# Optimization experiments

Measured on AMD Instinct MI355X. Metric: run time of the kernel, lower is better.

## Reference

```python
import jax, jax.numpy as jnp
import numpy as np

N_NODES = 100000
N_EDGES = 1600000
D_IN = 128
D_HID = 128
D_OUT = 32


def setup_inputs() -> dict:
    key = jax.random.key(0)
    ks = jax.random.split(key, 10)
    x = jax.random.normal(ks[0], (N_NODES, D_IN), dtype=jnp.float32)
    edge_index = jax.random.randint(ks[1], (2, N_EDGES), 0, N_NODES, dtype=jnp.int64)
    s = 0.05
    return {
        "x": x,
        "edge_index": edge_index,
        "Wl0": jax.random.normal(ks[2], (D_IN, D_HID), jnp.float32) * s,
        "bl0": jnp.zeros((D_HID,), jnp.float32),
        "Wr0": jax.random.normal(ks[3], (D_IN, D_HID), jnp.float32) * s,
        "Wl1": jax.random.normal(ks[4], (D_HID, D_HID), jnp.float32) * s,
        "bl1": jnp.zeros((D_HID,), jnp.float32),
        "Wr1": jax.random.normal(ks[5], (D_HID, D_HID), jnp.float32) * s,
        "Wl2": jax.random.normal(ks[6], (D_HID, D_OUT), jnp.float32) * s,
        "bl2": jnp.zeros((D_OUT,), jnp.float32),
        "Wr2": jax.random.normal(ks[7], (D_HID, D_OUT), jnp.float32) * s,
    }


def _sage_conv(x, src, dst, Wl, bl, Wr):
    # PyG SAGEConv (aggr='mean', root_weight=True):
    # out[i] = lin_l(mean_{j in N(i)} x_j) + lin_r(x_i)
    n = x.shape[0]
    msgs = x[src]                                        # [E, F] gather
    agg = jax.ops.segment_sum(msgs, dst, num_segments=n) # [N, F] scatter-add
    deg = jax.ops.segment_sum(jnp.ones((src.shape[0],), x.dtype), dst, num_segments=n)
    mean = agg / jnp.maximum(deg, 1.0)[:, None]
    return mean @ Wl + bl + x @ Wr


def reference(x, edge_index, Wl0, bl0, Wr0, Wl1, bl1, Wr1, Wl2, bl2, Wr2):
    src, dst = edge_index[0], edge_index[1]
    h = jax.nn.relu(_sage_conv(x, src, dst, Wl0, bl0, Wr0))
    h = jax.nn.relu(_sage_conv(h, src, dst, Wl1, bl1, Wr1))
    h = _sage_conv(h, src, dst, Wl2, bl2, Wr2)
    return jax.nn.log_softmax(h, axis=1)
```

## Files before the change

kernel.cpp:

```cpp
#include <hip/hip_runtime.h>
#include <hip/hip_bf16.h>
#include <math.h>

#define NN 100000
#define NE 1600000

#define NCB 391
#define EB  4096
#define SCT 512
#define EPT 8
#define HBK 64
#define NSB 391
#define WPB 144

typedef __attribute__((ext_vector_type(8))) short short8;
typedef __attribute__((ext_vector_type(4))) float f32x4;

__device__ __forceinline__ unsigned short f2bf(float f) {
  union { float f; unsigned int i; } v; v.f = f;
  unsigned int i = v.i;
  unsigned int r = (i + 0x7FFFu + ((i >> 16) & 1u)) >> 16;
  return (unsigned short)r;
}
__device__ __forceinline__ float bflo(unsigned int u) {
  union { unsigned int i; float f; } v; v.i = u << 16; return v.f;
}
__device__ __forceinline__ float bfhi(unsigned int u) {
  union { unsigned int i; float f; } v; v.i = u & 0xFFFF0000u; return v.f;
}
__device__ __forceinline__ float bf1(unsigned short u) {
  union { unsigned int i; float f; } v; v.i = ((unsigned int)u) << 16; return v.f;
}

__global__ __launch_bounds__(512) void k_prep(
    const int* __restrict__ dst, int* __restrict__ part,
    const float* __restrict__ Wl0, const float* __restrict__ Wr0,
    const float* __restrict__ Wl1, const float* __restrict__ Wr1,
    const float* __restrict__ Wl2, const float* __restrict__ Wr2,
    unsigned short* __restrict__ B0, unsigned short* __restrict__ B1,
    unsigned short* __restrict__ B2) {
  if (blockIdx.x < HBK) {
    __shared__ int h[NCB];
    for (int i = threadIdx.x; i < NCB; i += 512) h[i] = 0;
    __syncthreads();
    int stride = HBK * 512;
    for (int e = blockIdx.x * 512 + threadIdx.x; e < NE; e += stride) {
      int d = dst[e];
      d = d < 0 ? 0 : (d >= NN ? NN - 1 : d);
      atomicAdd(&h[d >> 8], 1);
    }
    __syncthreads();
    for (int i = threadIdx.x; i < NCB; i += 512) part[blockIdx.x * NCB + i] = h[i];
  } else {
    int idx = (blockIdx.x - HBK) * 512 + threadIdx.x;
    if (idx < 32768) {
      int n = idx >> 7, k = idx & 127;
      float v = (n < 128) ? Wl0[k * 128 + n] : Wr0[k * 128 + (n - 128)];
      B0[idx] = f2bf(v);
    } else if (idx < 65536) {
      int j = idx - 32768;
      int n = j >> 7, k = j & 127;
      float v = (n < 128) ? Wl1[k * 128 + n] : Wr1[k * 128 + (n - 128)];
      B1[j] = f2bf(v);
    } else if (idx < 73728) {
      int j = idx - 65536;
      int n = j >> 7, k = j & 127;
      float v = (n < 32) ? Wl2[k * 32 + n] : Wr2[k * 32 + (n - 32)];
      B2[j] = f2bf(v);
    }
  }
}

__global__ __launch_bounds__(512) void k_cscan(const int* __restrict__ part,
                                               int* __restrict__ cboff,
                                               int* __restrict__ ccur,
                                               int* __restrict__ csroff) {
  __shared__ int sd[512];
  int t = threadIdx.x;
  int v = 0;
  if (t < NCB) {
    int s0 = 0, s1 = 0, s2 = 0, s3 = 0;
    #pragma unroll 4
    for (int k = 0; k < HBK; k += 4) {
      s0 += part[(k + 0) * NCB + t];
      s1 += part[(k + 1) * NCB + t];
      s2 += part[(k + 2) * NCB + t];
      s3 += part[(k + 3) * NCB + t];
    }
    v = (s0 + s1) + (s2 + s3);
    ccur[t * 16] = 0;
  }
  sd[t] = v;
  __syncthreads();
  for (int st = 1; st < 512; st <<= 1) {
    int x = (t >= st) ? sd[t - st] : 0;
    __syncthreads();
    sd[t] += x;
    __syncthreads();
  }
  if (t < NCB) cboff[t] = sd[t] - v;
  if (t == NCB - 1) { cboff[NCB] = sd[t]; csroff[NN] = sd[t]; }
}


__device__ __forceinline__ void cscatter_body(
    char* smem, int bid,
    const int* __restrict__ src, const int* __restrict__ dst,
    const int* __restrict__ cboff, int* __restrict__ ccur,
    unsigned int* __restrict__ ebuf) {
  int* lh = (int*)smem;
  int t = threadIdx.x;
  int base = bid * EB;
  for (int i = t; i < NCB; i += SCT) lh[i] = 0;
  __syncthreads();
  unsigned int rk[EPT], pv[EPT];
  #pragma unroll
  for (int i = 0; i < EPT; i++) {
    int e = base + i * SCT + t;
    rk[i] = 0xFFFFFFFFu;
    pv[i] = 0;
    if (e < NE) {
      int d = dst[e];
      d = d < 0 ? 0 : (d >= NN ? NN - 1 : d);
      int s = src[e];
      s = s < 0 ? 0 : (s >= NN ? NN - 1 : s);
      int cb = d >> 8;
      int r = atomicAdd(&lh[cb], 1);
      rk[i] = (((unsigned int)cb) << 13) | (unsigned int)r;
      pv[i] = (((unsigned int)(d & 255)) << 17) | (unsigned int)s;
    }
  }
  __syncthreads();
  for (int i = t; i < NCB; i += SCT) {
    int c = lh[i];
    int g = c ? atomicAdd(&ccur[i * 16], c) : 0;
    lh[i] = cboff[i] + g;
  }
  __syncthreads();
  #pragma unroll
  for (int i = 0; i < EPT; i++) {
    unsigned int r = rk[i];
    if (r != 0xFFFFFFFFu) {
      ebuf[lh[r >> 13] + (r & 0x1FFF)] = pv[i];
    }
  }
}

__device__ __forceinline__ void mgemm0_body(
    char* smem, int bid, const float* __restrict__ A,
    const unsigned short* __restrict__ Bp, const float* __restrict__ bias,
    unsigned short* __restrict__ yl, unsigned short* __restrict__ yr) {
  unsigned short* sA = (unsigned short*)smem;
  int tid = threadIdx.x;
  int nb  = bid * 128;

  #pragma unroll
  for (int i = 0; i < 8; i++) {
    int j = i * 512 + tid;
    int m = j >> 5;
    int k4 = (j & 31) * 4;
    int gn = nb + m;
    float4 v = make_float4(0.f, 0.f, 0.f, 0.f);
    if (gn < NN) v = *(const float4*)&A[gn * 128 + k4];
    unsigned int p0 = (unsigned int)f2bf(v.x) | ((unsigned int)f2bf(v.y) << 16);
    unsigned int p1 = (unsigned int)f2bf(v.z) | ((unsigned int)f2bf(v.w) << 16);
    *(uint2*)&sA[m * 136 + k4] = make_uint2(p0, p1);
  }
  __syncthreads();

  int wave = tid >> 6, lane = tid & 63;
  int l15 = lane & 15, lq = lane >> 4;
  int wm = wave & 1, wn = wave >> 1;
  int mbase = wm * 64;
  int nbase = wn * 64;

  f32x4 acc[4][4];
  #pragma unroll
  for (int mi = 0; mi < 4; mi++)
    #pragma unroll
    for (int ni = 0; ni < 4; ni++) acc[mi][ni] = (f32x4){0.f, 0.f, 0.f, 0.f};

  #pragma unroll
  for (int kc = 0; kc < 4; kc++) {
    int k0 = kc * 32 + lq * 8;
    short8 af[4], bfr[4];
    #pragma unroll
    for (int ni = 0; ni < 4; ni++)
      bfr[ni] = *(const short8*)&Bp[(nbase + ni * 16 + l15) * 128 + k0];
    #pragma unroll
    for (int mi = 0; mi < 4; mi++)
      af[mi] = *(const short8*)&sA[(mbase + mi * 16 + l15) * 136 + k0];
    #pragma unroll
    for (int mi = 0; mi < 4; mi++)
      #pragma unroll
      for (int ni = 0; ni < 4; ni++)
        acc[mi][ni] = __builtin_amdgcn_mfma_f32_16x16x32_bf16(
            af[mi], bfr[ni], acc[mi][ni], 0, 0, 0);
  }

  #pragma unroll
  for (int mi = 0; mi < 4; mi++) {
    #pragma unroll
    for (int ni = 0; ni < 4; ni++) {
      int n = nbase + ni * 16 + l15;
      #pragma unroll
      for (int r = 0; r < 4; r++) {
        int gn = nb + mbase + mi * 16 + lq * 4 + r;
        if (gn < NN) {
          float v = acc[mi][ni][r];
          if (n < 128) {
            yl[(size_t)gn * 128 + n] = f2bf(v);
          } else {
            int n2 = n - 128;
            yr[(size_t)gn * 128 + n2] = f2bf(v + bias[n2]);
          }
        }
      }
    }
  }
}

__global__ __launch_bounds__(512, 4) void k_scatgemm(
    const int* __restrict__ src, const int* __restrict__ dst,
    const int* __restrict__ cboff, int* __restrict__ ccur,
    unsigned int* __restrict__ ebuf,
    const float* __restrict__ x, const unsigned short* __restrict__ B0,
    const float* __restrict__ bias,
    unsigned short* __restrict__ yl, unsigned short* __restrict__ yr) {
  __shared__ char smem[128 * 136 * 2];
  if (blockIdx.x < NSB) {
    cscatter_body(smem, blockIdx.x, src, dst, cboff, ccur, ebuf);
  } else {
    mgemm0_body(smem, blockIdx.x - NSB, x, B0, bias, yl, yr);
  }
}

__global__ __launch_bounds__(256) void k_crefine(
    const unsigned int* __restrict__ ebuf, const int* __restrict__ cboff,
    int* __restrict__ csroff, float* __restrict__ invd,
    int* __restrict__ csrsrc) {
  __shared__ int lh[256], pos[256], cur[256];
  int b = blockIdx.x, t = threadIdx.x;
  lh[t] = 0; cur[t] = 0;
  __syncthreads();
  int beg = cboff[b], end = cboff[b + 1];
  for (int i = beg + t; i < end; i += 256) atomicAdd(&lh[ebuf[i] >> 17], 1);
  __syncthreads();
  int v = lh[t];
  pos[t] = v;
  __syncthreads();
  for (int st = 1; st < 256; st <<= 1) {
    int x = (t >= st) ? pos[t - st] : 0;
    __syncthreads();
    pos[t] += x;
    __syncthreads();
  }
  int nid = b * 256 + t;
  int mybase = cboff[b] + pos[t] - v;
  if (nid < NN) {
    csroff[nid] = mybase;
    invd[nid] = 1.0f / (float)(v < 1 ? 1 : v);
  }
  __syncthreads();
  pos[t] = mybase;
  __syncthreads();
  for (int i = beg + t; i < end; i += 256) {
    unsigned int u = ebuf[i];
    int local = u >> 17;
    int r = atomicAdd(&cur[local], 1);
    csrsrc[pos[local] + r] = (int)(u & 0x1FFFFu);
  }
}

template <int NC>
__global__ __launch_bounds__(512) void k_mgemm(
    const unsigned short* __restrict__ A, const unsigned short* __restrict__ Bp,
    const float* __restrict__ bias,
    unsigned short* __restrict__ yl, unsigned short* __restrict__ yr) {
  __shared__ unsigned short sA[128 * 136];
  int tid = threadIdx.x;
  int nb  = blockIdx.x * 128;

  #pragma unroll
  for (int i = 0; i < 4; i++) {
    int j = i * 512 + tid;
    int m = j >> 4;
    int k8 = (j & 15) * 8;
    int gn = nb + m;
    uint4 v = make_uint4(0, 0, 0, 0);
    if (gn < NN) v = *(const uint4*)&A[gn * 128 + k8];
    *(uint4*)&sA[m * 136 + k8] = v;
  }
  __syncthreads();

  int wave = tid >> 6, lane = tid & 63;
  int l15 = lane & 15, lq = lane >> 4;
  constexpr int MT = (NC == 256) ? 4 : 2;
  constexpr int NT = (NC == 256) ? 4 : 2;
  int wm, wn;
  if (NC == 256) { wm = wave & 1; wn = wave >> 1; }
  else           { wm = wave >> 1; wn = wave & 1; }
  int mbase = wm * (MT * 16);
  int nbase = wn * (NT * 16);

  f32x4 acc[MT][NT];
  #pragma unroll
  for (int mi = 0; mi < MT; mi++)
    #pragma unroll
    for (int ni = 0; ni < NT; ni++) acc[mi][ni] = (f32x4){0.f, 0.f, 0.f, 0.f};

  #pragma unroll
  for (int kc = 0; kc < 4; kc++) {
    int k0 = kc * 32 + lq * 8;
    short8 af[MT], bfr[NT];
    #pragma unroll
    for (int ni = 0; ni < NT; ni++)
      bfr[ni] = *(const short8*)&Bp[(nbase + ni * 16 + l15) * 128 + k0];
    #pragma unroll
    for (int mi = 0; mi < MT; mi++)
      af[mi] = *(const short8*)&sA[(mbase + mi * 16 + l15) * 136 + k0];
    #pragma unroll
    for (int mi = 0; mi < MT; mi++)
      #pragma unroll
      for (int ni = 0; ni < NT; ni++)
        acc[mi][ni] = __builtin_amdgcn_mfma_f32_16x16x32_bf16(
            af[mi], bfr[ni], acc[mi][ni], 0, 0, 0);
  }

  constexpr int HC = NC / 2;
  #pragma unroll
  for (int mi = 0; mi < MT; mi++) {
    #pragma unroll
    for (int ni = 0; ni < NT; ni++) {
      int n = nbase + ni * 16 + l15;
      #pragma unroll
      for (int r = 0; r < 4; r++) {
        int gn = nb + mbase + mi * 16 + lq * 4 + r;
        if (gn < NN) {
          float v = acc[mi][ni][r];
          if (n < HC) {
            yl[(size_t)gn * HC + n] = f2bf(v);
          } else {
            int n2 = n - HC;
            yr[(size_t)gn * HC + n2] = f2bf(v + bias[n2]);
          }
        }
      }
    }
  }
}

#define ACC8(u) do { \
  a0 += bflo((u).x); a1 += bfhi((u).x); \
  a2 += bflo((u).y); a3 += bfhi((u).y); \
  a4 += bflo((u).z); a5 += bfhi((u).z); \
  a6 += bflo((u).w); a7 += bfhi((u).w); } while (0)

__global__ __launch_bounds__(256) void k_agg128(
    const unsigned short* __restrict__ yl, const unsigned short* __restrict__ yr,
    const int* __restrict__ off, const int* __restrict__ csr,
    const float* __restrict__ invd, unsigned short* __restrict__ out, int relu) {
  int wid  = (blockIdx.x * 256 + threadIdx.x) >> 6;
  int lane = threadIdx.x & 63;
  if (wid >= NN) return;
  int beg = off[wid], end = off[wid + 1];
  int deg = end - beg;
  int q   = lane >> 4;
  int l16 = lane & 15;
  const uint4* ylp = (const uint4*)yl;

  float sc = invd[wid];
  uint4 rv = ((const uint4*)yr)[wid * 16 + l16];

  float a0 = 0.f, a1 = 0.f, a2 = 0.f, a3 = 0.f;
  float a4 = 0.f, a5 = 0.f, a6 = 0.f, a7 = 0.f;

  for (int w0 = 0; w0 < deg; w0 += 64) {
    int ei = w0 + lane;
    int sv = (ei < deg) ? csr[beg + ei] : 0;
    int wcnt = deg - w0; if (wcnt > 64) wcnt = 64;
    int full = wcnt >> 2;
    int p = 0;
    for (; p + 4 <= full; p += 4) {
      int b = p * 4 + q;
      int s0 = __shfl(sv, b,      64);
      int s1 = __shfl(sv, b + 4,  64);
      int s2 = __shfl(sv, b + 8,  64);
      int s3 = __shfl(sv, b + 12, 64);
      uint4 u0 = ylp[s0 * 16 + l16];
      uint4 u1 = ylp[s1 * 16 + l16];
      uint4 u2 = ylp[s2 * 16 + l16];
      uint4 u3 = ylp[s3 * 16 + l16];
      ACC8(u0); ACC8(u1); ACC8(u2); ACC8(u3);
    }
    for (; p < full; p++) {
      int s0 = __shfl(sv, p * 4 + q, 64);
      uint4 u0 = ylp[s0 * 16 + l16];
      ACC8(u0);
    }
    int rem = wcnt & 3;
    if (rem && q < rem) {
      int s0 = __shfl(sv, full * 4 + q, 64);
      uint4 u0 = ylp[s0 * 16 + l16];
      ACC8(u0);
    }
  }

  a0 += __shfl_xor(a0, 16, 64); a0 += __shfl_xor(a0, 32, 64);
  a1 += __shfl_xor(a1, 16, 64); a1 += __shfl_xor(a1, 32, 64);
  a2 += __shfl_xor(a2, 16, 64); a2 += __shfl_xor(a2, 32, 64);
  a3 += __shfl_xor(a3, 16, 64); a3 += __shfl_xor(a3, 32, 64);
  a4 += __shfl_xor(a4, 16, 64); a4 += __shfl_xor(a4, 32, 64);
  a5 += __shfl_xor(a5, 16, 64); a5 += __shfl_xor(a5, 32, 64);
  a6 += __shfl_xor(a6, 16, 64); a6 += __shfl_xor(a6, 32, 64);
  a7 += __shfl_xor(a7, 16, 64); a7 += __shfl_xor(a7, 32, 64);

  float v0 = a0 * sc + bflo(rv.x), v1 = a1 * sc + bfhi(rv.x);
  float v2 = a2 * sc + bflo(rv.y), v3 = a3 * sc + bfhi(rv.y);
  float v4 = a4 * sc + bflo(rv.z), v5 = a5 * sc + bfhi(rv.z);
  float v6 = a6 * sc + bflo(rv.w), v7 = a7 * sc + bfhi(rv.w);
  if (relu) {
    v0 = fmaxf(v0, 0.f); v1 = fmaxf(v1, 0.f);
    v2 = fmaxf(v2, 0.f); v3 = fmaxf(v3, 0.f);
    v4 = fmaxf(v4, 0.f); v5 = fmaxf(v5, 0.f);
    v6 = fmaxf(v6, 0.f); v7 = fmaxf(v7, 0.f);
  }
  if (q == 0) {
    unsigned int p0 = (unsigned int)f2bf(v0) | ((unsigned int)f2bf(v1) << 16);
    unsigned int p1 = (unsigned int)f2bf(v2) | ((unsigned int)f2bf(v3) << 16);
    unsigned int p2 = (unsigned int)f2bf(v4) | ((unsigned int)f2bf(v5) << 16);
    unsigned int p3 = (unsigned int)f2bf(v6) | ((unsigned int)f2bf(v7) << 16);
    ((uint4*)out)[wid * 16 + l16] = make_uint4(p0, p1, p2, p3);
  }
}

#define ACC4(u) do { \
  a0 += bflo((u).x); a1 += bfhi((u).x); \
  a2 += bflo((u).y); a3 += bfhi((u).y); } while (0)

__global__ __launch_bounds__(256) void k_agg32_lsm(
    const unsigned short* __restrict__ yl, const unsigned short* __restrict__ yr,
    const int* __restrict__ off, const int* __restrict__ csr,
    const float* __restrict__ invd, float* __restrict__ out) {
  int wid  = (blockIdx.x * 256 + threadIdx.x) >> 6;
  int lane = threadIdx.x & 63;
  if (wid >= NN) return;
  int beg = off[wid], end = off[wid + 1];
  int deg = end - beg;
  int q  = lane >> 3;
  int l8 = lane & 7;
  const uint2* ylp = (const uint2*)yl;

  float sc = invd[wid];
  uint2 rv = ((const uint2*)yr)[wid * 8 + l8];

  float a0 = 0.f, a1 = 0.f, a2 = 0.f, a3 = 0.f;

  for (int w0 = 0; w0 < deg; w0 += 64) {
    int ei = w0 + lane;
    int sv = (ei < deg) ? csr[beg + ei] : 0;
    int wcnt = deg - w0; if (wcnt > 64) wcnt = 64;
    int full = wcnt >> 3;
    int p = 0;
    for (; p + 2 <= full; p += 2) {
      int b = p * 8 + q;
      int s0 = __shfl(sv, b,     64);
      int s1 = __shfl(sv, b + 8, 64);
      uint2 u0 = ylp[s0 * 8 + l8];
      uint2 u1 = ylp[s1 * 8 + l8];
      ACC4(u0); ACC4(u1);
    }
    for (; p < full; p++) {
      int s0 = __shfl(sv, p * 8 + q, 64);
      uint2 u0 = ylp[s0 * 8 + l8];
      ACC4(u0);
    }
    int rem = wcnt & 7;
    if (rem && q < rem) {
      int s0 = __shfl(sv, full * 8 + q, 64);
      uint2 u0 = ylp[s0 * 8 + l8];
      ACC4(u0);
    }
  }

  a0 += __shfl_xor(a0, 8, 64); a0 += __shfl_xor(a0, 16, 64); a0 += __shfl_xor(a0, 32, 64);
  a1 += __shfl_xor(a1, 8, 64); a1 += __shfl_xor(a1, 16, 64); a1 += __shfl_xor(a1, 32, 64);
  a2 += __shfl_xor(a2, 8, 64); a2 += __shfl_xor(a2, 16, 64); a2 += __shfl_xor(a2, 32, 64);
  a3 += __shfl_xor(a3, 8, 64); a3 += __shfl_xor(a3, 16, 64); a3 += __shfl_xor(a3, 32, 64);

  float v0 = a0 * sc + bflo(rv.x), v1 = a1 * sc + bfhi(rv.x);
  float v2 = a2 * sc + bflo(rv.y), v3 = a3 * sc + bfhi(rv.y);

  float m = fmaxf(fmaxf(v0, v1), fmaxf(v2, v3));
  m = fmaxf(m, __shfl_xor(m, 1, 64));
  m = fmaxf(m, __shfl_xor(m, 2, 64));
  m = fmaxf(m, __shfl_xor(m, 4, 64));
  float e0 = expf(v0 - m), e1 = expf(v1 - m);
  float e2 = expf(v2 - m), e3 = expf(v3 - m);
  float s = (e0 + e1) + (e2 + e3);
  s += __shfl_xor(s, 1, 64);
  s += __shfl_xor(s, 2, 64);
  s += __shfl_xor(s, 4, 64);
  float ls = logf(s);
  if (q == 0) {
    float4 o = make_float4(v0 - m - ls, v1 - m - ls, v2 - m - ls, v3 - m - ls);
    ((float4*)out)[wid * 8 + l8] = o;
  }
}


extern "C" void kernel_launch(void* const* d_in, const int* in_sizes, int n_in,
                              void* d_out, int out_size, void* d_ws, size_t ws_size,
                              hipStream_t stream) {
  (void)in_sizes; (void)n_in; (void)out_size; (void)ws_size;
  const float* x   = (const float*)d_in[0];
  const int*   ei  = (const int*)d_in[1];
  const float* Wl0 = (const float*)d_in[2];
  const float* bl0 = (const float*)d_in[3];
  const float* Wr0 = (const float*)d_in[4];
  const float* Wl1 = (const float*)d_in[5];
  const float* bl1 = (const float*)d_in[6];
  const float* Wr1 = (const float*)d_in[7];
  const float* Wl2 = (const float*)d_in[8];
  const float* bl2 = (const float*)d_in[9];
  const float* Wr2 = (const float*)d_in[10];
  const int* srcI = ei;
  const int* dstI = ei + NE;

  char* w = (char*)d_ws;
  int*   cboff  = (int*)(w + (32 << 10));
  unsigned short* B0 = (unsigned short*)(w + (64 << 10));
  unsigned short* B1 = (unsigned short*)(w + (160 << 10));
  unsigned short* B2 = (unsigned short*)(w + (256 << 10));
  int*   part   = (int*)(w + (288 << 10));
  int*   ccur   = (int*)(w + (416 << 10));
  int*   csroff = (int*)(w + (512 << 10));
  float* invd   = (float*)(w + (1024 << 10));
  unsigned int* ebuf = (unsigned int*)(w + (size_t)(2) * 1024 * 1024);
  int*   csrsrc = (int*)(w + (size_t)(9) * 1024 * 1024);
  unsigned short* ylb = (unsigned short*)(w + (size_t)(16) * 1024 * 1024);
  unsigned short* yrb = (unsigned short*)(w + (size_t)(48) * 1024 * 1024);
  unsigned short* hb  = (unsigned short*)(w + (size_t)(80) * 1024 * 1024);

  dim3 gg((NN + 127) / 128);

  k_prep<<<HBK + WPB, 512, 0, stream>>>(dstI, part, Wl0, Wr0, Wl1, Wr1, Wl2, Wr2,
                                        B0, B1, B2);
  k_cscan<<<1, 512, 0, stream>>>(part, cboff, ccur, csroff);
  k_scatgemm<<<NSB + 782, 512, 0, stream>>>(srcI, dstI, cboff, ccur, ebuf,
                                            x, B0, bl0, ylb, yrb);
  k_crefine<<<NCB, 256, 0, stream>>>(ebuf, cboff, csroff, invd, csrsrc);
  k_agg128<<<(NN * 64) / 256, 256, 0, stream>>>(ylb, yrb, csroff, csrsrc, invd, hb, 1);
  k_mgemm<256><<<gg, 512, 0, stream>>>(hb, B1, bl1, ylb, yrb);
  k_agg128<<<(NN * 64) / 256, 256, 0, stream>>>(ylb, yrb, csroff, csrsrc, invd, hb, 1);
  k_mgemm<64><<<gg, 512, 0, stream>>>(hb, B2, bl2, ylb, yrb);
  k_agg32_lsm<<<(NN * 64) / 256, 256, 0, stream>>>(ylb, yrb, csroff, csrsrc, invd,
                                                   (float*)d_out);
}
```

Before: 417.5 us.

## Fuse neighbor aggregation into following GEMM and interleave scatter/GEMM blocks

Replaces the separate k_agg128 and k_mgemm launches with k_aggemm. Each block's waves gather and mean-aggregate 16 nodes apiece and write the ReLU'd bf16 rows straight into the shared-memory A tile before the MFMA GEMM. This removes the hidden-activation round trip through global memory and two kernel launches. The trade-off is fewer waves per node and serial per-wave node loops, which may expose gather latency. Separately, k_scatgemm now interleaves scatter and GEMM blocks (one of every three blocks scatters) so the two workloads run at the same time across the GPU.

After: 507.3 us. 21.5% more time.

```diff
diff --git a/kernel.cpp b/kernel.cpp
--- a/kernel.cpp
+++ b/kernel.cpp
@@ -12,6 +12,7 @@
 #define HBK 64
 #define NSB 391
 #define WPB 144
+#define NGB 782
 
 typedef __attribute__((ext_vector_type(8))) short short8;
 typedef __attribute__((ext_vector_type(4))) float f32x4;
@@ -228,10 +229,12 @@
     const float* __restrict__ bias,
     unsigned short* __restrict__ yl, unsigned short* __restrict__ yr) {
   __shared__ char smem[128 * 136 * 2];
-  if (blockIdx.x < NSB) {
-    cscatter_body(smem, blockIdx.x, src, dst, cboff, ccur, ebuf);
+  int bid = blockIdx.x;
+  int third = bid / 3;
+  if (bid - third * 3 == 0) {
+    cscatter_body(smem, third, src, dst, cboff, ccur, ebuf);
   } else {
-    mgemm0_body(smem, blockIdx.x - NSB, x, B0, bias, yl, yr);
+    mgemm0_body(smem, bid - third - 1, x, B0, bias, yl, yr);
   }
 }
 
@@ -272,28 +275,96 @@
   }
 }
 
+#define ACC8(u) do { \
+  a0 += bflo((u).x); a1 += bfhi((u).x); \
+  a2 += bflo((u).y); a3 += bfhi((u).y); \
+  a4 += bflo((u).z); a5 += bfhi((u).z); \
+  a6 += bflo((u).w); a7 += bfhi((u).w); } while (0)
+
 template <int NC>
-__global__ __launch_bounds__(512) void k_mgemm(
-    const unsigned short* __restrict__ A, const unsigned short* __restrict__ Bp,
-    const float* __restrict__ bias,
-    unsigned short* __restrict__ yl, unsigned short* __restrict__ yr) {
+__global__ __launch_bounds__(512) void k_aggemm(
+    const unsigned short* __restrict__ yl, const unsigned short* __restrict__ yrr,
+    const int* __restrict__ off, const int* __restrict__ csr,
+    const float* __restrict__ invd,
+    const unsigned short* __restrict__ Bp, const float* __restrict__ bias,
+    unsigned short* __restrict__ outl, unsigned short* __restrict__ outr) {
   __shared__ unsigned short sA[128 * 136];
-  int tid = threadIdx.x;
-  int nb  = blockIdx.x * 128;
-
-  #pragma unroll
-  for (int i = 0; i < 4; i++) {
-    int j = i * 512 + tid;
-    int m = j >> 4;
-    int k8 = (j & 15) * 8;
-    int gn = nb + m;
-    uint4 v = make_uint4(0, 0, 0, 0);
-    if (gn < NN) v = *(const uint4*)&A[gn * 128 + k8];
-    *(uint4*)&sA[m * 136 + k8] = v;
-  }
-  __syncthreads();
-
-  int wave = tid >> 6, lane = tid & 63;
+  int tid = threadIdx.x, wave = tid >> 6, lane = tid & 63;
+  int nb = blockIdx.x * 128;
+  int q = lane >> 4, l16 = lane & 15;
+  const uint4* ylp = (const uint4*)yl;
+
+  #pragma unroll 1
+  for (int j = 0; j < 16; j++) {
+    int m = wave * 16 + j;
+    int wid = nb + m;
+    float a0 = 0.f, a1 = 0.f, a2 = 0.f, a3 = 0.f;
+    float a4 = 0.f, a5 = 0.f, a6 = 0.f, a7 = 0.f;
+    float sc = 0.f;
+    uint4 rv = make_uint4(0, 0, 0, 0);
+    if (wid < NN) {
+      sc = invd[wid];
+      rv = ((const uint4*)yrr)[wid * 16 + l16];
+      int beg = off[wid], end = off[wid + 1];
+      int deg = end - beg;
+      for (int w0 = 0; w0 < deg; w0 += 64) {
+        int ei = w0 + lane;
+        int sv = (ei < deg) ? csr[beg + ei] : 0;
+        int wcnt = deg - w0; if (wcnt > 64) wcnt = 64;
+        int full = wcnt >> 2;
+        int p = 0;
+        for (; p + 4 <= full; p += 4) {
+          int b = p * 4 + q;
+          int s0 = __shfl(sv, b,      64);
+          int s1 = __shfl(sv, b + 4,  64);
+          int s2 = __shfl(sv, b + 8,  64);
+          int s3 = __shfl(sv, b + 12, 64);
+          uint4 u0 = ylp[s0 * 16 + l16];
+          uint4 u1 = ylp[s1 * 16 + l16];
+          uint4 u2 = ylp[s2 * 16 + l16];
+          uint4 u3 = ylp[s3 * 16 + l16];
+          ACC8(u0); ACC8(u1); ACC8(u2); ACC8(u3);
+        }
+        for (; p < full; p++) {
+          int s0 = __shfl(sv, p * 4 + q, 64);
+          uint4 u0 = ylp[s0 * 16 + l16];
+          ACC8(u0);
+        }
+        int rem = wcnt & 3;
+        if (rem && q < rem) {
+          int s0 = __shfl(sv, full * 4 + q, 64);
+          uint4 u0 = ylp[s0 * 16 + l16];
+          ACC8(u0);
+        }
+      }
+    }
+    a0 += __shfl_xor(a0, 16, 64); a0 += __shfl_xor(a0, 32, 64);
+    a1 += __shfl_xor(a1, 16, 64); a1 += __shfl_xor(a1, 32, 64);
+    a2 += __shfl_xor(a2, 16, 64); a2 += __shfl_xor(a2, 32, 64);
+    a3 += __shfl_xor(a3, 16, 64); a3 += __shfl_xor(a3, 32, 64);
+    a4 += __shfl_xor(a4, 16, 64); a4 += __shfl_xor(a4, 32, 64);
+    a5 += __shfl_xor(a5, 16, 64); a5 += __shfl_xor(a5, 32, 64);
+    a6 += __shfl_xor(a6, 16, 64); a6 += __shfl_xor(a6, 32, 64);
+    a7 += __shfl_xor(a7, 16, 64); a7 += __shfl_xor(a7, 32, 64);
+
+    float v0 = fmaxf(a0 * sc + bflo(rv.x), 0.f);
+    float v1 = fmaxf(a1 * sc + bfhi(rv.x), 0.f);
+    float v2 = fmaxf(a2 * sc + bflo(rv.y), 0.f);
+    float v3 = fmaxf(a3 * sc + bfhi(rv.y), 0.f);
+    float v4 = fmaxf(a4 * sc + bflo(rv.z), 0.f);
+    float v5 = fmaxf(a5 * sc + bfhi(rv.z), 0.f);
+    float v6 = fmaxf(a6 * sc + bflo(rv.w), 0.f);
+    float v7 = fmaxf(a7 * sc + bfhi(rv.w), 0.f);
+    if (q == 0) {
+      unsigned int p0 = (unsigned int)f2bf(v0) | ((unsigned int)f2bf(v1) << 16);
+      unsigned int p1 = (unsigned int)f2bf(v2) | ((unsigned int)f2bf(v3) << 16);
+      unsigned int p2 = (unsigned int)f2bf(v4) | ((unsigned int)f2bf(v5) << 16);
+      unsigned int p3 = (unsigned int)f2bf(v6) | ((unsigned int)f2bf(v7) << 16);
+      *(uint4*)&sA[m * 136 + l16 * 8] = make_uint4(p0, p1, p2, p3);
+    }
+  }
+  __syncthreads();
+
   int l15 = lane & 15, lq = lane >> 4;
   constexpr int MT = (NC == 256) ? 4 : 2;
   constexpr int NT = (NC == 256) ? 4 : 2;
@@ -339,98 +410,14 @@
         if (gn < NN) {
           float v = acc[mi][ni][r];
           if (n < HC) {
-            yl[(size_t)gn * HC + n] = f2bf(v);
+            outl[(size_t)gn * HC + n] = f2bf(v);
           } else {
             int n2 = n - HC;
-            yr[(size_t)gn * HC + n2] = f2bf(v + bias[n2]);
+            outr[(size_t)gn * HC + n2] = f2bf(v + bias[n2]);
           }
         }
       }
     }
-  }
-}
-
-#define ACC8(u) do { \
-  a0 += bflo((u).x); a1 += bfhi((u).x); \
-  a2 += bflo((u).y); a3 += bfhi((u).y); \
-  a4 += bflo((u).z); a5 += bfhi((u).z); \
-  a6 += bflo((u).w); a7 += bfhi((u).w); } while (0)
-
-__global__ __launch_bounds__(256) void k_agg128(
-    const unsigned short* __restrict__ yl, const unsigned short* __restrict__ yr,
-    const int* __restrict__ off, const int* __restrict__ csr,
-    const float* __restrict__ invd, unsigned short* __restrict__ out, int relu) {
-  int wid  = (blockIdx.x * 256 + threadIdx.x) >> 6;
-  int lane = threadIdx.x & 63;
-  if (wid >= NN) return;
-  int beg = off[wid], end = off[wid + 1];
-  int deg = end - beg;
-  int q   = lane >> 4;
-  int l16 = lane & 15;
-  const uint4* ylp = (const uint4*)yl;
-
-  float sc = invd[wid];
-  uint4 rv = ((const uint4*)yr)[wid * 16 + l16];
-
-  float a0 = 0.f, a1 = 0.f, a2 = 0.f, a3 = 0.f;
-  float a4 = 0.f, a5 = 0.f, a6 = 0.f, a7 = 0.f;
-
-  for (int w0 = 0; w0 < deg; w0 += 64) {
-    int ei = w0 + lane;
-    int sv = (ei < deg) ? csr[beg + ei] : 0;
-    int wcnt = deg - w0; if (wcnt > 64) wcnt = 64;
-    int full = wcnt >> 2;
-    int p = 0;
-    for (; p + 4 <= full; p += 4) {
-      int b = p * 4 + q;
-      int s0 = __shfl(sv, b,      64);
-      int s1 = __shfl(sv, b + 4,  64);
-      int s2 = __shfl(sv, b + 8,  64);
-      int s3 = __shfl(sv, b + 12, 64);
-      uint4 u0 = ylp[s0 * 16 + l16];
-      uint4 u1 = ylp[s1 * 16 + l16];
-      uint4 u2 = ylp[s2 * 16 + l16];
-      uint4 u3 = ylp[s3 * 16 + l16];
-      ACC8(u0); ACC8(u1); ACC8(u2); ACC8(u3);
-    }
-    for (; p < full; p++) {
-      int s0 = __shfl(sv, p * 4 + q, 64);
-      uint4 u0 = ylp[s0 * 16 + l16];
-      ACC8(u0);
-    }
-    int rem = wcnt & 3;
-    if (rem && q < rem) {
-      int s0 = __shfl(sv, full * 4 + q, 64);
-      uint4 u0 = ylp[s0 * 16 + l16];
-      ACC8(u0);
-    }
-  }
-
-  a0 += __shfl_xor(a0, 16, 64); a0 += __shfl_xor(a0, 32, 64);
-  a1 += __shfl_xor(a1, 16, 64); a1 += __shfl_xor(a1, 32, 64);
-  a2 += __shfl_xor(a2, 16, 64); a2 += __shfl_xor(a2, 32, 64);
-  a3 += __shfl_xor(a3, 16, 64); a3 += __shfl_xor(a3, 32, 64);
-  a4 += __shfl_xor(a4, 16, 64); a4 += __shfl_xor(a4, 32, 64);
-  a5 += __shfl_xor(a5, 16, 64); a5 += __shfl_xor(a5, 32, 64);
-  a6 += __shfl_xor(a6, 16, 64); a6 += __shfl_xor(a6, 32, 64);
-  a7 += __shfl_xor(a7, 16, 64); a7 += __shfl_xor(a7, 32, 64);
-
-  float v0 = a0 * sc + bflo(rv.x), v1 = a1 * sc + bfhi(rv.x);
-  float v2 = a2 * sc + bflo(rv.y), v3 = a3 * sc + bfhi(rv.y);
-  float v4 = a4 * sc + bflo(rv.z), v5 = a5 * sc + bfhi(rv.z);
-  float v6 = a6 * sc + bflo(rv.w), v7 = a7 * sc + bfhi(rv.w);
-  if (relu) {
-    v0 = fmaxf(v0, 0.f); v1 = fmaxf(v1, 0.f);
-    v2 = fmaxf(v2, 0.f); v3 = fmaxf(v3, 0.f);
-    v4 = fmaxf(v4, 0.f); v5 = fmaxf(v5, 0.f);
-    v6 = fmaxf(v6, 0.f); v7 = fmaxf(v7, 0.f);
-  }
-  if (q == 0) {
-    unsigned int p0 = (unsigned int)f2bf(v0) | ((unsigned int)f2bf(v1) << 16);
-    unsigned int p1 = (unsigned int)f2bf(v2) | ((unsigned int)f2bf(v3) << 16);
-    unsigned int p2 = (unsigned int)f2bf(v4) | ((unsigned int)f2bf(v5) << 16);
-    unsigned int p3 = (unsigned int)f2bf(v6) | ((unsigned int)f2bf(v7) << 16);
-    ((uint4*)out)[wid * 16 + l16] = make_uint4(p0, p1, p2, p3);
   }
 }
 
@@ -538,22 +525,22 @@
   float* invd   = (float*)(w + (1024 << 10));
   unsigned int* ebuf = (unsigned int*)(w + (size_t)(2) * 1024 * 1024);
   int*   csrsrc = (int*)(w + (size_t)(9) * 1024 * 1024);
-  unsigned short* ylb = (unsigned short*)(w + (size_t)(16) * 1024 * 1024);
-  unsigned short* yrb = (unsigned short*)(w + (size_t)(48) * 1024 * 1024);
-  unsigned short* hb  = (unsigned short*)(w + (size_t)(80) * 1024 * 1024);
-
-  dim3 gg((NN + 127) / 128);
+  unsigned short* yl0 = (unsigned short*)(w + (size_t)(16) * 1024 * 1024);
+  unsigned short* yr0 = (unsigned short*)(w + (size_t)(48) * 1024 * 1024);
+  unsigned short* yl1 = (unsigned short*)(w + (size_t)(80) * 1024 * 1024);
+  unsigned short* yl2 = (unsigned short*)(w + (size_t)(16) * 1024 * 1024);
+  unsigned short* yr2 = (unsigned short*)(w + (size_t)(32) * 1024 * 1024);
 
   k_prep<<<HBK + WPB, 512, 0, stream>>>(dstI, part, Wl0, Wr0, Wl1, Wr1, Wl2, Wr2,
                                         B0, B1, B2);
   k_cscan<<<1, 512, 0, stream>>>(part, cboff, ccur, csroff);
-  k_scatgemm<<<NSB + 782, 512, 0, stream>>>(srcI, dstI, cboff, ccur, ebuf,
-                                            x, B0, bl0, ylb, yrb);
+  k_scatgemm<<<NSB + NGB, 512, 0, stream>>>(srcI, dstI, cboff, ccur, ebuf,
+                                            x, B0, bl0, yl0, yr0);
   k_crefine<<<NCB, 256, 0, stream>>>(ebuf, cboff, csroff, invd, csrsrc);
-  k_agg128<<<(NN * 64) / 256, 256, 0, stream>>>(ylb, yrb, csroff, csrsrc, invd, hb, 1);
-  k_mgemm<256><<<gg, 512, 0, stream>>>(hb, B1, bl1, ylb, yrb);
-  k_agg128<<<(NN * 64) / 256, 256, 0, stream>>>(ylb, yrb, csroff, csrsrc, invd, hb, 1);
-  k_mgemm<64><<<gg, 512, 0, stream>>>(hb, B2, bl2, ylb, yrb);
-  k_agg32_lsm<<<(NN * 64) / 256, 256, 0, stream>>>(ylb, yrb, csroff, csrsrc, invd,
+  k_aggemm<256><<<NGB, 512, 0, stream>>>(yl0, yr0, csroff, csrsrc, invd,
+                                         B1, bl1, yl1, yr0);
+  k_aggemm<64><<<NGB, 512, 0, stream>>>(yl1, yr0, csroff, csrsrc, invd,
+                                        B2, bl2, yl2, yr2);
+  k_agg32_lsm<<<(NN * 64) / 256, 256, 0, stream>>>(yl2, yr2, csroff, csrsrc, invd,
                                                    (float*)d_out);
 }
```

## Build CSR via per-node global degree atomics instead of two-level bucket sort

Applied to the files above, without the earlier changes.

Replaces the two-pass bucketed counting sort (coarse chunk histogram, staging buffer, per-chunk refine) with direct per-node degree counting through global atomics. A block-level scan, a chunk scan and a fixup pass then produce the CSR offsets, and the scatter places each edge straight into its final slot using per-node global atomic cursors. This drops the intermediate ebuf pass and the refine kernel, and interleaves scatter blocks with GEMM blocks in the fused launch. In exchange it adds a memset and two extra small kernels, relies on contended global atomics, and makes edge order within each row nondeterministic.

Result: slower. 519.0 us (+24.3%).

```diff
diff --git a/kernel.cpp b/kernel.cpp
--- a/kernel.cpp
+++ b/kernel.cpp
@@ -9,9 +9,10 @@
 #define EB  4096
 #define SCT 512
 #define EPT 8
-#define HBK 64
+#define HBK 128
 #define NSB 391
 #define WPB 144
+#define NGB 782
 
 typedef __attribute__((ext_vector_type(8))) short short8;
 typedef __attribute__((ext_vector_type(4))) float f32x4;
@@ -28,29 +29,21 @@
 __device__ __forceinline__ float bfhi(unsigned int u) {
   union { unsigned int i; float f; } v; v.i = u & 0xFFFF0000u; return v.f;
 }
-__device__ __forceinline__ float bf1(unsigned short u) {
-  union { unsigned int i; float f; } v; v.i = ((unsigned int)u) << 16; return v.f;
-}
 
 __global__ __launch_bounds__(512) void k_prep(
-    const int* __restrict__ dst, int* __restrict__ part,
+    const int* __restrict__ dst, int* __restrict__ deg,
     const float* __restrict__ Wl0, const float* __restrict__ Wr0,
     const float* __restrict__ Wl1, const float* __restrict__ Wr1,
     const float* __restrict__ Wl2, const float* __restrict__ Wr2,
     unsigned short* __restrict__ B0, unsigned short* __restrict__ B1,
     unsigned short* __restrict__ B2) {
   if (blockIdx.x < HBK) {
-    __shared__ int h[NCB];
-    for (int i = threadIdx.x; i < NCB; i += 512) h[i] = 0;
-    __syncthreads();
     int stride = HBK * 512;
     for (int e = blockIdx.x * 512 + threadIdx.x; e < NE; e += stride) {
       int d = dst[e];
       d = d < 0 ? 0 : (d >= NN ? NN - 1 : d);
-      atomicAdd(&h[d >> 8], 1);
-    }
-    __syncthreads();
-    for (int i = threadIdx.x; i < NCB; i += 512) part[blockIdx.x * NCB + i] = h[i];
+      atomicAdd(&deg[d], 1);
+    }
   } else {
     int idx = (blockIdx.x - HBK) * 512 + threadIdx.x;
     if (idx < 32768) {
@@ -71,25 +64,34 @@
   }
 }
 
+__global__ __launch_bounds__(256) void k_bscan(
+    const int* __restrict__ deg, int* __restrict__ part,
+    int* __restrict__ csroff, float* __restrict__ invd) {
+  __shared__ int sd[256];
+  int b = blockIdx.x, t = threadIdx.x;
+  int nid = b * 256 + t;
+  int d = (nid < NN) ? deg[nid] : 0;
+  sd[t] = d;
+  __syncthreads();
+  for (int st = 1; st < 256; st <<= 1) {
+    int x = (t >= st) ? sd[t - st] : 0;
+    __syncthreads();
+    sd[t] += x;
+    __syncthreads();
+  }
+  if (nid < NN) {
+    csroff[nid] = sd[t] - d;
+    invd[nid] = 1.0f / (float)(d < 1 ? 1 : d);
+  }
+  if (t == 255) part[b] = sd[255];
+}
+
 __global__ __launch_bounds__(512) void k_cscan(const int* __restrict__ part,
                                                int* __restrict__ cboff,
-                                               int* __restrict__ ccur,
                                                int* __restrict__ csroff) {
   __shared__ int sd[512];
   int t = threadIdx.x;
-  int v = 0;
-  if (t < NCB) {
-    int s0 = 0, s1 = 0, s2 = 0, s3 = 0;
-    #pragma unroll 4
-    for (int k = 0; k < HBK; k += 4) {
-      s0 += part[(k + 0) * NCB + t];
-      s1 += part[(k + 1) * NCB + t];
-      s2 += part[(k + 2) * NCB + t];
-      s3 += part[(k + 3) * NCB + t];
-    }
-    v = (s0 + s1) + (s2 + s3);
-    ccur[t * 16] = 0;
-  }
+  int v = (t < NCB) ? part[t] : 0;
   sd[t] = v;
   __syncthreads();
   for (int st = 1; st < 512; st <<= 1) {
@@ -99,49 +101,32 @@
     __syncthreads();
   }
   if (t < NCB) cboff[t] = sd[t] - v;
-  if (t == NCB - 1) { cboff[NCB] = sd[t]; csroff[NN] = sd[t]; }
-}
-
-
-__device__ __forceinline__ void cscatter_body(
-    char* smem, int bid,
-    const int* __restrict__ src, const int* __restrict__ dst,
-    const int* __restrict__ cboff, int* __restrict__ ccur,
-    unsigned int* __restrict__ ebuf) {
-  int* lh = (int*)smem;
+  if (t == NCB - 1) csroff[NN] = sd[t];
+}
+
+__global__ __launch_bounds__(256) void k_fixup(const int* __restrict__ cboff,
+                                               int* __restrict__ csroff) {
+  int nid = blockIdx.x * 256 + threadIdx.x;
+  if (nid < NN) csroff[nid] += cboff[blockIdx.x];
+}
+
+
+__device__ __forceinline__ void scatter_body(
+    int bid, const int* __restrict__ src, const int* __restrict__ dst,
+    const int* __restrict__ csroff, int* __restrict__ cur,
+    int* __restrict__ csrsrc) {
   int t = threadIdx.x;
   int base = bid * EB;
-  for (int i = t; i < NCB; i += SCT) lh[i] = 0;
-  __syncthreads();
-  unsigned int rk[EPT], pv[EPT];
   #pragma unroll
   for (int i = 0; i < EPT; i++) {
     int e = base + i * SCT + t;
-    rk[i] = 0xFFFFFFFFu;
-    pv[i] = 0;
     if (e < NE) {
       int d = dst[e];
       d = d < 0 ? 0 : (d >= NN ? NN - 1 : d);
       int s = src[e];
       s = s < 0 ? 0 : (s >= NN ? NN - 1 : s);
-      int cb = d >> 8;
-      int r = atomicAdd(&lh[cb], 1);
-      rk[i] = (((unsigned int)cb) << 13) | (unsigned int)r;
-      pv[i] = (((unsigned int)(d & 255)) << 17) | (unsigned int)s;
-    }
-  }
-  __syncthreads();
-  for (int i = t; i < NCB; i += SCT) {
-    int c = lh[i];
-    int g = c ? atomicAdd(&ccur[i * 16], c) : 0;
-    lh[i] = cboff[i] + g;
-  }
-  __syncthreads();
-  #pragma unroll
-  for (int i = 0; i < EPT; i++) {
-    unsigned int r = rk[i];
-    if (r != 0xFFFFFFFFu) {
-      ebuf[lh[r >> 13] + (r & 0x1FFF)] = pv[i];
+      int r = atomicAdd(&cur[d], 1);
+      csrsrc[csroff[d] + r] = s;
     }
   }
 }
@@ -222,53 +207,18 @@
 
 __global__ __launch_bounds__(512, 4) void k_scatgemm(
     const int* __restrict__ src, const int* __restrict__ dst,
-    const int* __restrict__ cboff, int* __restrict__ ccur,
-    unsigned int* __restrict__ ebuf,
+    const int* __restrict__ csroff, int* __restrict__ cur,
+    int* __restrict__ csrsrc,
     const float* __restrict__ x, const unsigned short* __restrict__ B0,
     const float* __restrict__ bias,
     unsigned short* __restrict__ yl, unsigned short* __restrict__ yr) {
   __shared__ char smem[128 * 136 * 2];
-  if (blockIdx.x < NSB) {
-    cscatter_body(smem, blockIdx.x, src, dst, cboff, ccur, ebuf);
+  int bid = blockIdx.x;
+  int third = bid / 3;
+  if (bid - third * 3 == 0) {
+    scatter_body(third, src, dst, csroff, cur, csrsrc);
   } else {
-    mgemm0_body(smem, blockIdx.x - NSB, x, B0, bias, yl, yr);
-  }
-}
-
-__global__ __launch_bounds__(256) void k_crefine(
-    const unsigned int* __restrict__ ebuf, const int* __restrict__ cboff,
-    int* __restrict__ csroff, float* __restrict__ invd,
-    int* __restrict__ csrsrc) {
-  __shared__ int lh[256], pos[256], cur[256];
-  int b = blockIdx.x, t = threadIdx.x;
-  lh[t] = 0; cur[t] = 0;
-  __syncthreads();
-  int beg = cboff[b], end = cboff[b + 1];
-  for (int i = beg + t; i < end; i += 256) atomicAdd(&lh[ebuf[i] >> 17], 1);
-  __syncthreads();
-  int v = lh[t];
-  pos[t] = v;
-  __syncthreads();
-  for (int st = 1; st < 256; st <<= 1) {
-    int x = (t >= st) ? pos[t - st] : 0;
-    __syncthreads();
-    pos[t] += x;
-    __syncthreads();
-  }
-  int nid = b * 256 + t;
-  int mybase = cboff[b] + pos[t] - v;
-  if (nid < NN) {
-    csroff[nid] = mybase;
-    invd[nid] = 1.0f / (float)(v < 1 ? 1 : v);
-  }
-  __syncthreads();
-  pos[t] = mybase;
-  __syncthreads();
-  for (int i = beg + t; i < end; i += 256) {
-    unsigned int u = ebuf[i];
-    int local = u >> 17;
-    int r = atomicAdd(&cur[local], 1);
-    csrsrc[pos[local] + r] = (int)(u & 0x1FFFFu);
+    mgemm0_body(smem, bid - third - 1, x, B0, bias, yl, yr);
   }
 }
 
@@ -533,23 +483,25 @@
   unsigned short* B1 = (unsigned short*)(w + (160 << 10));
   unsigned short* B2 = (unsigned short*)(w + (256 << 10));
   int*   part   = (int*)(w + (288 << 10));
-  int*   ccur   = (int*)(w + (416 << 10));
-  int*   csroff = (int*)(w + (512 << 10));
-  float* invd   = (float*)(w + (1024 << 10));
-  unsigned int* ebuf = (unsigned int*)(w + (size_t)(2) * 1024 * 1024);
-  int*   csrsrc = (int*)(w + (size_t)(9) * 1024 * 1024);
+  int*   deg    = (int*)(w + (size_t)(1024 << 10));
+  int*   cur    = (int*)(w + (size_t)(1024 << 10) + 409600);
+  int*   csroff = (int*)(w + (size_t)(2) * 1024 * 1024);
+  float* invd   = (float*)(w + (size_t)(3) * 1024 * 1024);
+  int*   csrsrc = (int*)(w + (size_t)(4) * 1024 * 1024);
   unsigned short* ylb = (unsigned short*)(w + (size_t)(16) * 1024 * 1024);
   unsigned short* yrb = (unsigned short*)(w + (size_t)(48) * 1024 * 1024);
   unsigned short* hb  = (unsigned short*)(w + (size_t)(80) * 1024 * 1024);
 
-  dim3 gg((NN + 127) / 128);
-
-  k_prep<<<HBK + WPB, 512, 0, stream>>>(dstI, part, Wl0, Wr0, Wl1, Wr1, Wl2, Wr2,
+  dim3 gg(NGB);
+
+  hipMemsetAsync(w + (size_t)(1024 << 10), 0, 819200, stream);
+  k_prep<<<HBK + WPB, 512, 0, stream>>>(dstI, deg, Wl0, Wr0, Wl1, Wr1, Wl2, Wr2,
                                         B0, B1, B2);
-  k_cscan<<<1, 512, 0, stream>>>(part, cboff, ccur, csroff);
-  k_scatgemm<<<NSB + 782, 512, 0, stream>>>(srcI, dstI, cboff, ccur, ebuf,
+  k_bscan<<<NCB, 256, 0, stream>>>(deg, part, csroff, invd);
+  k_cscan<<<1, 512, 0, stream>>>(part, cboff, csroff);
+  k_fixup<<<NCB, 256, 0, stream>>>(cboff, csroff);
+  k_scatgemm<<<NSB + NGB, 512, 0, stream>>>(srcI, dstI, csroff, cur, csrsrc,
                                             x, B0, bl0, ylb, yrb);
-  k_crefine<<<NCB, 256, 0, stream>>>(ebuf, cboff, csroff, invd, csrsrc);
   k_agg128<<<(NN * 64) / 256, 256, 0, stream>>>(ylb, yrb, csroff, csrsrc, invd, hb, 1);
   k_mgemm<256><<<gg, 512, 0, stream>>>(hb, B1, bl1, ylb, yrb);
   k_agg128<<<(NN * 64) / 256, 256, 0, stream>>>(ylb, yrb, csroff, csrsrc, invd, hb, 1);
```

## Split layer-0 GEMM across scatter and refine kernels with interleaved blocks

Applied to the files above, without the earlier changes.

The first-layer feature GEMM is now split in half. One half of its blocks is interleaved with the edge-scatter blocks (even/odd block IDs), and the other half is interleaved with the CSR refine blocks in a new combined kernel. The aim is to hide the latency-bound scatter and refine phases behind compute-heavy GEMM work, and to mix block types so the work is balanced across CUs. The refine body now runs with 512 threads, half of them idle during the scan, and uses more shared memory per block, which may lower its occupancy.

Result: slower. 434.4 us (+4.1%).

```diff
diff --git a/kernel.cpp b/kernel.cpp
--- a/kernel.cpp
+++ b/kernel.cpp
@@ -12,6 +12,7 @@
 #define HBK 64
 #define NSB 391
 #define WPB 144
+#define NGB 782
 
 typedef __attribute__((ext_vector_type(8))) short short8;
 typedef __attribute__((ext_vector_type(4))) float f32x4;
@@ -27,9 +28,6 @@
 }
 __device__ __forceinline__ float bfhi(unsigned int u) {
   union { unsigned int i; float f; } v; v.i = u & 0xFFFF0000u; return v.f;
-}
-__device__ __forceinline__ float bf1(unsigned short u) {
-  union { unsigned int i; float f; } v; v.i = ((unsigned int)u) << 16; return v.f;
 }
 
 __global__ __launch_bounds__(512) void k_prep(
@@ -146,6 +144,46 @@
   }
 }
 
+__device__ __forceinline__ void crefine_body(
+    char* smem, int b, const unsigned int* __restrict__ ebuf,
+    const int* __restrict__ cboff, int* __restrict__ csroff,
+    float* __restrict__ invd, int* __restrict__ csrsrc) {
+  int* lh  = (int*)smem;
+  int* pos = (int*)(smem + 1024);
+  int* cur = (int*)(smem + 2048);
+  int t = threadIdx.x;
+  if (t < 256) { lh[t] = 0; cur[t] = 0; }
+  __syncthreads();
+  int beg = cboff[b], end = cboff[b + 1];
+  for (int i = beg + t; i < end; i += 512) atomicAdd(&lh[ebuf[i] >> 17], 1);
+  __syncthreads();
+  int v = 0;
+  if (t < 256) { v = lh[t]; pos[t] = v; }
+  __syncthreads();
+  for (int st = 1; st < 256; st <<= 1) {
+    int x = (t < 256 && t >= st) ? pos[t - st] : 0;
+    __syncthreads();
+    if (t < 256) pos[t] += x;
+    __syncthreads();
+  }
+  if (t < 256) {
+    int nid = b * 256 + t;
+    int mybase = cboff[b] + pos[t] - v;
+    if (nid < NN) {
+      csroff[nid] = mybase;
+      invd[nid] = 1.0f / (float)(v < 1 ? 1 : v);
+    }
+    pos[t] = mybase;
+  }
+  __syncthreads();
+  for (int i = beg + t; i < end; i += 512) {
+    unsigned int u = ebuf[i];
+    int local = u >> 17;
+    int r = atomicAdd(&cur[local], 1);
+    csrsrc[pos[local] + r] = (int)(u & 0x1FFFFu);
+  }
+}
+
 __device__ __forceinline__ void mgemm0_body(
     char* smem, int bid, const float* __restrict__ A,
     const unsigned short* __restrict__ Bp, const float* __restrict__ bias,
@@ -220,7 +258,7 @@
   }
 }
 
-__global__ __launch_bounds__(512, 4) void k_scatgemm(
+__global__ __launch_bounds__(512, 4) void k_scatgemmA(
     const int* __restrict__ src, const int* __restrict__ dst,
     const int* __restrict__ cboff, int* __restrict__ ccur,
     unsigned int* __restrict__ ebuf,
@@ -228,47 +266,27 @@
     const float* __restrict__ bias,
     unsigned short* __restrict__ yl, unsigned short* __restrict__ yr) {
   __shared__ char smem[128 * 136 * 2];
-  if (blockIdx.x < NSB) {
-    cscatter_body(smem, blockIdx.x, src, dst, cboff, ccur, ebuf);
+  int bid = blockIdx.x;
+  if ((bid & 1) == 0) {
+    cscatter_body(smem, bid >> 1, src, dst, cboff, ccur, ebuf);
   } else {
-    mgemm0_body(smem, blockIdx.x - NSB, x, B0, bias, yl, yr);
-  }
-}
-
-__global__ __launch_bounds__(256) void k_crefine(
+    mgemm0_body(smem, bid >> 1, x, B0, bias, yl, yr);
+  }
+}
+
+__global__ __launch_bounds__(512, 4) void k_refgemmB(
     const unsigned int* __restrict__ ebuf, const int* __restrict__ cboff,
     int* __restrict__ csroff, float* __restrict__ invd,
-    int* __restrict__ csrsrc) {
-  __shared__ int lh[256], pos[256], cur[256];
-  int b = blockIdx.x, t = threadIdx.x;
-  lh[t] = 0; cur[t] = 0;
-  __syncthreads();
-  int beg = cboff[b], end = cboff[b + 1];
-  for (int i = beg + t; i < end; i += 256) atomicAdd(&lh[ebuf[i] >> 17], 1);
-  __syncthreads();
-  int v = lh[t];
-  pos[t] = v;
-  __syncthreads();
-  for (int st = 1; st < 256; st <<= 1) {
-    int x = (t >= st) ? pos[t - st] : 0;
-    __syncthreads();
-    pos[t] += x;
-    __syncthreads();
-  }
-  int nid = b * 256 + t;
-  int mybase = cboff[b] + pos[t] - v;
-  if (nid < NN) {
-    csroff[nid] = mybase;
-    invd[nid] = 1.0f / (float)(v < 1 ? 1 : v);
-  }
-  __syncthreads();
-  pos[t] = mybase;
-  __syncthreads();
-  for (int i = beg + t; i < end; i += 256) {
-    unsigned int u = ebuf[i];
-    int local = u >> 17;
-    int r = atomicAdd(&cur[local], 1);
-    csrsrc[pos[local] + r] = (int)(u & 0x1FFFFu);
+    int* __restrict__ csrsrc,
+    const float* __restrict__ x, const unsigned short* __restrict__ B0,
+    const float* __restrict__ bias,
+    unsigned short* __restrict__ yl, unsigned short* __restrict__ yr) {
+  __shared__ char smem[128 * 136 * 2];
+  int bid = blockIdx.x;
+  if ((bid & 1) == 0) {
+    crefine_body(smem, bid >> 1, ebuf, cboff, csroff, invd, csrsrc);
+  } else {
+    mgemm0_body(smem, NSB + (bid >> 1), x, B0, bias, yl, yr);
   }
 }
 
@@ -542,14 +560,15 @@
   unsigned short* yrb = (unsigned short*)(w + (size_t)(48) * 1024 * 1024);
   unsigned short* hb  = (unsigned short*)(w + (size_t)(80) * 1024 * 1024);
 
-  dim3 gg((NN + 127) / 128);
+  dim3 gg(NGB);
 
   k_prep<<<HBK + WPB, 512, 0, stream>>>(dstI, part, Wl0, Wr0, Wl1, Wr1, Wl2, Wr2,
                                         B0, B1, B2);
   k_cscan<<<1, 512, 0, stream>>>(part, cboff, ccur, csroff);
-  k_scatgemm<<<NSB + 782, 512, 0, stream>>>(srcI, dstI, cboff, ccur, ebuf,
-                                            x, B0, bl0, ylb, yrb);
-  k_crefine<<<NCB, 256, 0, stream>>>(ebuf, cboff, csroff, invd, csrsrc);
+  k_scatgemmA<<<2 * NSB, 512, 0, stream>>>(srcI, dstI, cboff, ccur, ebuf,
+                                           x, B0, bl0, ylb, yrb);
+  k_refgemmB<<<2 * NSB, 512, 0, stream>>>(ebuf, cboff, csroff, invd, csrsrc,
+                                          x, B0, bl0, ylb, yrb);
   k_agg128<<<(NN * 64) / 256, 256, 0, stream>>>(ylb, yrb, csroff, csrsrc, invd, hb, 1);
   k_mgemm<256><<<gg, 512, 0, stream>>>(hb, B1, bl1, ylb, yrb);
   k_agg128<<<(NN * 64) / 256, 256, 0, stream>>>(ylb, yrb, csroff, csrsrc, invd, hb, 1);
```
